# Performance work log

Hardware: AMD Instinct MI355X
Metric: run time of the kernel (lower is better)

The kernel has to match this reference:

```python
import jax, jax.numpy as jnp
import numpy as np

N_NODES = 100000
N_EDGES = 1600000
N_GRAPHS = 64
D = 128


def gcn_conv(x, W, b, src, dst, num_nodes):
    # PyG GCNConv: x' = D^{-1/2} (A + I) D^{-1/2} (X W) + b
    h = x @ W  # [N, H]
    deg = jax.ops.segment_sum(jnp.ones_like(dst, dtype=h.dtype), dst,
                              num_segments=num_nodes)  # includes self-loop (>=1)
    dinv = jax.lax.rsqrt(deg)
    norm = dinv[src] * dinv[dst]  # [E+N]
    msg = h[src] * norm[:, None]  # gather + scale
    out = jax.ops.segment_sum(msg, dst, num_segments=num_nodes)
    return out + b


def setup_inputs() -> dict:
    key = jax.random.key(0)
    ks = jax.random.split(key, 10)
    x = jax.random.normal(ks[0], (N_NODES, D), dtype=jnp.float32)
    edge_index = jax.random.randint(ks[1], (2, N_EDGES), 0, N_NODES, dtype=jnp.int64)
    batch = jnp.sort(jax.random.randint(ks[2], (N_NODES,), 0, N_GRAPHS, dtype=jnp.int64))
    s = 1.0 / np.sqrt(D)
    W1 = jax.random.normal(ks[3], (D, D), dtype=jnp.float32) * s
    b1 = jnp.zeros((D,), dtype=jnp.float32)
    W2 = jax.random.normal(ks[4], (D, D), dtype=jnp.float32) * s
    b2 = jnp.zeros((D,), dtype=jnp.float32)
    Wfc = jax.random.normal(ks[5], (D, D), dtype=jnp.float32) * s
    bfc = jnp.zeros((D,), dtype=jnp.float32)
    return {"x": x, "edge_index": edge_index, "batch": batch,
            "W1": W1, "b1": b1, "W2": W2, "b2": b2, "Wfc": Wfc, "bfc": bfc}


def reference(x, edge_index, batch, W1, b1, W2, b2, Wfc, bfc):
    num_nodes = x.shape[0]
    # add self-loops (PyG default add_self_loops=True)
    loop = jnp.arange(num_nodes, dtype=edge_index.dtype)
    src = jnp.concatenate([edge_index[0], loop])
    dst = jnp.concatenate([edge_index[1], loop])

    h = jax.nn.relu(gcn_conv(x, W1, b1, src, dst, num_nodes))
    h = jax.nn.relu(gcn_conv(h, W2, b2, src, dst, num_nodes))

    # global_mean_pool over graph segment ids
    sums = jax.ops.segment_sum(h, batch, num_segments=N_GRAPHS)
    cnts = jax.ops.segment_sum(jnp.ones((num_nodes,), h.dtype), batch,
                               num_segments=N_GRAPHS)
    pooled = sums / jnp.maximum(cnts, 1.0)[:, None]

    return jax.nn.relu(pooled @ Wfc + bfc)
```

## Files before the change

kernel.cpp:

```cpp
#include <hip/hip_runtime.h>
#include <hip/hip_bf16.h>
#include <stdint.h>

typedef unsigned int uint;
typedef unsigned short ushort;
typedef __attribute__((ext_vector_type(8))) short short8;
typedef __attribute__((ext_vector_type(4))) float floatx4;

#define DD 128
#define BSHIFT 9
#define NBLK 256

__device__ __forceinline__ float bf2f(ushort h){ return __uint_as_float(((uint)h)<<16); }
__device__ __forceinline__ ushort f2bf(float f){
    uint u = __float_as_uint(f);
    u += 0x7fffu + ((u>>16)&1u);
    return (ushort)(u>>16);
}

__global__ void k_detect(const int* ei, const ushort* x, const ushort* W1, int* flags){
    int t = threadIdx.x;
    unsigned long long b0 = __ballot((t < 32) ? (ei[2*t+1] == 0) : 1);
    uint ex = (((uint)x[2*t])  >> 7) & 0xffu;
    uint ew = (((uint)W1[2*t]) >> 7) & 0xffu;
    unsigned long long b1 = __ballot(ex >= 90u && ex <= 160u);
    unsigned long long b2 = __ballot(ew >= 90u && ew <= 160u);
    if (t == 0){
        flags[0] = (b0 == ~0ull) ? 1 : 0;
        flags[1] = (__popcll(b1) >= 48) ? 1 : 0;
        flags[2] = (__popcll(b2) >= 48) ? 1 : 0;
    }
}

__global__ void k_canon(const void* s0,const void* s1,const void* s2,
                        const void* s3,const void* s4,const void* s5,
                        float* d0,float* d1,float* d2,float* d3,float* d4,float* d5,
                        ushort* wb1, ushort* wb2,
                        const int* flags){
    int f = flags[2];
    int i = blockIdx.x*blockDim.x + threadIdx.x;
    const void* s; float* d; int off; int r;
    if (i < 49152){
        r = i>>14; off = i & 16383;
        s = (r==0)?s0:((r==1)?s1:s2);
        d = (r==0)?d0:((r==1)?d1:d2);
    } else {
        int j = i - 49152; r = j>>7; off = j & 127;
        if (r >= 3) return;
        s = (r==0)?s3:((r==1)?s4:s5);
        d = (r==0)?d3:((r==1)?d4:d5);
        d[off] = f ? bf2f(((const ushort*)s)[off]) : ((const float*)s)[off];
        return;
    }
    float val = f ? bf2f(((const ushort*)s)[off]) : ((const float*)s)[off];
    d[off] = val;
    if (r < 2){
        int k = off>>7, n = off&127;
        int c = n>>4, nn = n&15, kk = k>>5, q = (k>>3)&3, j = k&7;
        ushort* wb = (r==0) ? wb1 : wb2;
        wb[((c*4+kk)*64 + q*16 + nn)*8 + j] = f2bf(val);
    }
}

__global__ void k_init(float* pooled, int PM, int* buktot, int nbuk){
    int i = blockIdx.x*blockDim.x + threadIdx.x;
    if (i < PM) pooled[i] = 0.f;
    if (i < nbuk) buktot[i] = 0;
}

__global__ __launch_bounds__(256) void k_hist(const int* __restrict__ ei,
                                              const int* __restrict__ flags,
                                              int* __restrict__ ghist,
                                              int* __restrict__ buktot,
                                              int E, int nbuk, int chunk){
    __shared__ int lh[1024];
    int f = flags[0];
    int t = threadIdx.x, b = blockIdx.x;
    for (int i=t;i<nbuk;i+=256) lh[i]=0;
    __syncthreads();
    int e0 = b*chunk, e1 = min(E, e0+chunk);
    for (int e=e0+t; e<e1; e+=256){
        int d = f ? ei[2*(E+e)] : ei[E+e];
        atomicAdd(&lh[d>>BSHIFT],1);
    }
    __syncthreads();
    for (int i=t;i<nbuk;i+=256){
        int v = lh[i];
        ghist[i*NBLK + b] = v;
        if (v) atomicAdd(&buktot[i], v);
    }
}

__global__ void k_scanB2(const int* __restrict__ buktot, int* __restrict__ bukoff, int nbuk){
    __shared__ int ts[256];
    int t = threadIdx.x;
    int v = (t<nbuk) ? buktot[t] : 0;
    ts[t] = v; __syncthreads();
    for (int off=1; off<256; off<<=1){
        int x = (t>=off) ? ts[t-off] : 0;
        __syncthreads(); ts[t] += x; __syncthreads();
    }
    if (t<nbuk) bukoff[t] = ts[t] - v;
}

__global__ __launch_bounds__(256) void k_apply(const int* __restrict__ ghist,
                                               const int* __restrict__ bukoff,
                                               int* __restrict__ gstart, int nbuk){
    __shared__ int ts[256];
    int b = blockIdx.x, t = threadIdx.x;
    int v = ghist[b*NBLK + t];
    ts[t] = v; __syncthreads();
    for (int off=1; off<256; off<<=1){
        int x = (t>=off) ? ts[t-off] : 0;
        __syncthreads(); ts[t] += x; __syncthreads();
    }
    gstart[b*NBLK + t] = bukoff[b] + ts[t] - v;
}

__global__ __launch_bounds__(256) void k_scat(const int* __restrict__ ei,
                                              const int* __restrict__ flags,
                                              const int* __restrict__ gstart,
                                              uint2* __restrict__ pairs,
                                              int E, int nbuk, int chunk){
    __shared__ int cur[1024];
    int f = flags[0];
    int t = threadIdx.x, b = blockIdx.x;
    for (int i=t;i<nbuk;i+=256) cur[i] = gstart[i*NBLK + b];
    __syncthreads();
    int e0 = b*chunk, e1 = min(E, e0+chunk);
    for (int e=e0+t; e<e1; e+=256){
        int d = f ? ei[2*(E+e)] : ei[E+e];
        int s = f ? ei[2*e]     : ei[e];
        int p = atomicAdd(&cur[d>>BSHIFT],1);
        pairs[p] = make_uint2((uint)s,(uint)d);
    }
}

__global__ __launch_bounds__(256) void k_build(const uint2* __restrict__ pairs,
                                               const int* __restrict__ gstart,
                                               int* __restrict__ rowptr,
                                               float* __restrict__ dinv,
                                               int* __restrict__ srcb,
                                               int E, int nbuk, int M){
    __shared__ int cnt[512], off[512], cur[512], ps[256];
    int b = blockIdx.x, t = threadIdx.x;
    int base = gstart[b*NBLK];
    int end  = (b+1<nbuk) ? gstart[(b+1)*NBLK] : E;
    for (int i=t;i<512;i+=256) cnt[i]=0;
    __syncthreads();
    for (int e=base+t; e<end; e+=256){
        uint2 pr = pairs[e];
        atomicAdd(&cnt[pr.y & 511],1);
    }
    __syncthreads();
    int c0 = cnt[2*t], c1 = cnt[2*t+1];
    int s = c0+c1;
    ps[t]=s; __syncthreads();
    for (int o2=1;o2<256;o2<<=1){
        int x=(t>=o2)?ps[t-o2]:0; __syncthreads(); ps[t]+=x; __syncthreads();
    }
    int ex = ps[t]-s;
    off[2*t]=ex;    off[2*t+1]=ex+c0;
    cur[2*t]=ex;    cur[2*t+1]=ex+c0;
    __syncthreads();
    for (int i=t;i<512;i+=256){
        int n = (b<<BSHIFT)+i;
        if (n<M){
            rowptr[n] = base + off[i];
            dinv[n]   = rsqrtf((float)(cnt[i]+1));
        }
    }
    if (b==0 && t==0) rowptr[M] = E;
    for (int e=base+t; e<end; e+=256){
        uint2 pr = pairs[e];
        int i = pr.y & 511;
        int p = atomicAdd(&cur[i],1);
        srcb[base+p] = (int)pr.x;
    }
}

__global__ __launch_bounds__(256) void k_gemm(const ushort* __restrict__ Xb,
                                              const float* __restrict__ Xf,
                                              const ushort* __restrict__ Wb,
                                              const float* __restrict__ dinv,
                                              const int* __restrict__ flags, int force_bf16,
                                              ushort* __restrict__ Hp, int M){
    __shared__ uint4 Xs4[1024];
    __shared__ uint4 Ws4[2048];
    int t = threadIdx.x;
    int n0 = blockIdx.x*64;
    int xbf = force_bf16 ? 1 : flags[1];

    {
        const uint4* sW = (const uint4*)Wb;
        #pragma unroll
        for (int j=0;j<8;j++) Ws4[t + j*256] = sW[t + j*256];
    }
    #pragma unroll
    for (int g=0; g<4; g++){
        int u = g*256 + t;
        int row = u>>4, kk = (u>>2)&3, q = u&3;
        int n = n0 + row;
        uint4 o;
        if (n < M){
            if (xbf){
                o = *(const uint4*)(Xb + (size_t)n*DD + kk*32 + q*8);
            } else {
                const float* p = Xf + (size_t)n*DD + kk*32 + q*8;
                float4 a = *(const float4*)p;
                float4 b = *(const float4*)(p+4);
                o.x = (uint)f2bf(a.x) | ((uint)f2bf(a.y)<<16);
                o.y = (uint)f2bf(a.z) | ((uint)f2bf(a.w)<<16);
                o.z = (uint)f2bf(b.x) | ((uint)f2bf(b.y)<<16);
                o.w = (uint)f2bf(b.z) | ((uint)f2bf(b.w)<<16);
            }
        } else { o = make_uint4(0,0,0,0); }
        int w = row>>4, m16 = row&15;
        Xs4[(w*4+kk)*64 + q*16 + m16] = o;
    }
    __syncthreads();

    int wv = t>>6, lane = t&63;
    const ushort* Xs = (const ushort*)Xs4;
    const ushort* Ws = (const ushort*)Ws4;

    floatx4 acc[8];
    #pragma unroll
    for (int c=0;c<8;c++) acc[c] = (floatx4){0.f,0.f,0.f,0.f};

    #pragma unroll
    for (int kk=0;kk<4;kk++){
        short8 af = *(const short8*)(Xs + ((size_t)((wv*4+kk)*64 + lane))*8);
        #pragma unroll
        for (int c=0;c<8;c++){
            short8 bf = *(const short8*)(Ws + ((size_t)((c*4+kk)*64 + lane))*8);
            acc[c] = __builtin_amdgcn_mfma_f32_16x16x32_bf16(af, bf, acc[c], 0, 0, 0);
        }
    }

    int quad = lane>>4, col = lane&15;
    int rbase = n0 + wv*16 + quad*4;
    float dv[4];
    #pragma unroll
    for (int r=0;r<4;r++) dv[r] = (rbase + r < M) ? dinv[rbase + r] : 0.f;
    #pragma unroll
    for (int c=0;c<8;c++){
        #pragma unroll
        for (int r=0;r<4;r++){
            int gn = rbase + r;
            if (gn < M) Hp[(size_t)gn*DD + c*16 + col] = f2bf(acc[c][r]*dv[r]);
        }
    }
}

__global__ __launch_bounds__(256) void k_gather(const ushort* __restrict__ Hp,
                                                const int* __restrict__ rowptr,
                                                const int* __restrict__ srcb,
                                                const float* __restrict__ dinv,
                                                const float* __restrict__ bc,
                                                ushort* __restrict__ Xout, int M){
    int wid  = (int)((blockIdx.x*(size_t)blockDim.x + threadIdx.x) >> 6);
    int lane = threadIdx.x & 63;
    if (wid >= M) return;
    int q   = lane >> 4;
    int l16 = lane & 15;
    const uint4* Hp4 = (const uint4*)Hp;

    float acc[8];
    #pragma unroll
    for (int c=0;c<8;c++) acc[c] = 0.f;

    #define ACCUM(vv) { \
        acc[0] += __uint_as_float((vv).x<<16); acc[1] += __uint_as_float((vv).x&0xffff0000u); \
        acc[2] += __uint_as_float((vv).y<<16); acc[3] += __uint_as_float((vv).y&0xffff0000u); \
        acc[4] += __uint_as_float((vv).z<<16); acc[5] += __uint_as_float((vv).z&0xffff0000u); \
        acc[6] += __uint_as_float((vv).w<<16); acc[7] += __uint_as_float((vv).w&0xffff0000u); }

    int rp  = rowptr[wid];
    int rp1 = rowptr[wid+1];
    int total = (rp1 - rp) + 1;
    int j = 0;
    while (j < total){
        int m = total - j; if (m > 64) m = 64;
        int pos = j + lane;
        int idx = wid;
        if (lane < m && pos > 0) idx = srcb[rp + pos - 1];
        for (int g = 0; g < m; g += 8){
            int r0 = g + q, r1 = g + 4 + q;
            int s0 = __shfl(idx, r0, 64);
            int s1 = __shfl(idx, r1, 64);
            uint4 v0 = make_uint4(0,0,0,0), v1 = make_uint4(0,0,0,0);
            if (r0 < m) v0 = Hp4[(size_t)s0*16 + l16];
            if (r1 < m) v1 = Hp4[(size_t)s1*16 + l16];
            ACCUM(v0);
            ACCUM(v1);
        }
        j += m;
    }
    #undef ACCUM

    #pragma unroll
    for (int c=0;c<8;c++){
        acc[c] += __shfl_xor(acc[c], 16, 64);
        acc[c] += __shfl_xor(acc[c], 32, 64);
    }

    if (lane < 16){
        float w = dinv[wid];
        const float* bp = bc + l16*8;
        uint4 o;
        float r0,r1;
        r0 = fmaxf(fmaf(acc[0], w, bp[0]), 0.f);
        r1 = fmaxf(fmaf(acc[1], w, bp[1]), 0.f);
        o.x = (uint)f2bf(r0) | ((uint)f2bf(r1)<<16);
        r0 = fmaxf(fmaf(acc[2], w, bp[2]), 0.f);
        r1 = fmaxf(fmaf(acc[3], w, bp[3]), 0.f);
        o.y = (uint)f2bf(r0) | ((uint)f2bf(r1)<<16);
        r0 = fmaxf(fmaf(acc[4], w, bp[4]), 0.f);
        r1 = fmaxf(fmaf(acc[5], w, bp[5]), 0.f);
        o.z = (uint)f2bf(r0) | ((uint)f2bf(r1)<<16);
        r0 = fmaxf(fmaf(acc[6], w, bp[6]), 0.f);
        r1 = fmaxf(fmaf(acc[7], w, bp[7]), 0.f);
        o.w = (uint)f2bf(r0) | ((uint)f2bf(r1)<<16);
        ((uint4*)Xout)[(size_t)wid*16 + l16] = o;
    }
}

__global__ __launch_bounds__(256) void k_pool(const ushort* __restrict__ X3,
                                              const int* __restrict__ batch,
                                              const int* __restrict__ flags,
                                              float* __restrict__ pooled, int M){
    int f = flags[0];
    int t = threadIdx.x;
    int c32 = t & 63;
    int row = t >> 6;
    int n0 = blockIdx.x * 256;
    if (n0 >= M) return;
    int nend = n0 + 256; if (nend > M) nend = M;
    const uint* X3u = (const uint*)X3;

    float a0 = 0.f, a1 = 0.f;
    int cur = -1;

    int n = n0 + row;
    #define POOL_PROC(gg, uu) \
        if ((gg) != cur){ \
            if (cur >= 0){ \
                atomicAdd(&pooled[cur*DD + 2*c32],   a0); \
                atomicAdd(&pooled[cur*DD + 2*c32+1], a1); \
            } \
            a0 = 0.f; a1 = 0.f; cur = (gg); \
        } \
        a0 += __uint_as_float((uu)<<16); \
        a1 += __uint_as_float((uu) & 0xffff0000u);

    for (; n + 12 < nend; n += 16){
        int g0 = f ? batch[2*n]      : batch[n];
        int g1 = f ? batch[2*(n+4)]  : batch[n+4];
        int g2 = f ? batch[2*(n+8)]  : batch[n+8];
        int g3 = f ? batch[2*(n+12)] : batch[n+12];
        uint u0 = X3u[(size_t)n*64      + c32];
        uint u1 = X3u[(size_t)(n+4)*64  + c32];
        uint u2 = X3u[(size_t)(n+8)*64  + c32];
        uint u3 = X3u[(size_t)(n+12)*64 + c32];
        POOL_PROC(g0, u0);
        POOL_PROC(g1, u1);
        POOL_PROC(g2, u2);
        POOL_PROC(g3, u3);
    }
    for (; n < nend; n += 4){
        int g = f ? batch[2*n] : batch[n];
        uint u = X3u[(size_t)n*64 + c32];
        POOL_PROC(g, u);
    }
    #undef POOL_PROC

    if (cur >= 0){
        atomicAdd(&pooled[cur*DD + 2*c32],   a0);
        atomicAdd(&pooled[cur*DD + 2*c32+1], a1);
    }
}

__global__ void k_cnt(const int* __restrict__ batch, const int* __restrict__ flags,
                      float* __restrict__ cntf, int M, int G){
    int f = flags[0];
    int g = blockIdx.x*blockDim.x + threadIdx.x;
    if (g >= G) return;
    int lo = 0, hi = M;
    while (lo < hi){ int mid = (lo+hi)>>1; int bv = f ? batch[2*mid] : batch[mid]; if (bv > g) hi = mid; else lo = mid+1; }
    int ub_g = lo;
    lo = 0; hi = M;
    while (lo < hi){ int mid = (lo+hi)>>1; int bv = f ? batch[2*mid] : batch[mid]; if (bv > g-1) hi = mid; else lo = mid+1; }
    cntf[g] = (float)(ub_g - lo);
}

__global__ void k_fc(const float* __restrict__ pooled, const float* __restrict__ cntf,
                     const float* __restrict__ Wcf, const float* __restrict__ bcf,
                     const int* __restrict__ flags, ushort* out16, float* out32){
    __shared__ float p[128];
    int g = blockIdx.x, c = threadIdx.x;
    p[c] = pooled[g*DD + c] / fmaxf(cntf[g], 1.f);
    __syncthreads();
    float acc = bcf[c];
    #pragma unroll 8
    for (int k=0;k<128;k++) acc = fmaf(p[k], Wcf[k*DD + c], acc);
    float r = fmaxf(acc, 0.f);
    if (flags[1]) out16[g*DD + c] = f2bf(r);
    else          out32[g*DD + c] = r;
}

extern "C" void kernel_launch(void* const* d_in, const int* in_sizes, int n_in,
                              void* d_out, int out_size, void* d_ws, size_t ws_size,
                              hipStream_t stream) {
    const void* x    = d_in[0];
    const int*  ei   = (const int*)d_in[1];
    const int*  bat  = (const int*)d_in[2];
    const void* W1   = d_in[3];
    const void* b1   = d_in[4];
    const void* W2   = d_in[5];
    const void* b2   = d_in[6];
    const void* Wfc  = d_in[7];
    const void* bfc  = d_in[8];

    int M = in_sizes[0] / DD;
    int E = in_sizes[1] / 2;
    int G = out_size / DD;
    int nbuk  = (M + 511) >> BSHIFT;
    int chunk = (E + NBLK - 1) / NBLK;

    char* w = (char*)d_ws;
    auto alloc = [&](size_t bytes)->void*{ void* p = (void*)w; w += (bytes + 255) & ~(size_t)255; return p; };
    int*    flags  = (int*)   alloc(16);
    int*    rowptr = (int*)   alloc((size_t)(M+1)*4);
    int*    ghist  = (int*)   alloc((size_t)nbuk*NBLK*4);
    int*    gstart = (int*)   alloc((size_t)nbuk*NBLK*4);
    int*    buktot = (int*)   alloc((size_t)nbuk*4);
    int*    bukoff = (int*)   alloc((size_t)nbuk*4);
    float*  dinv   = (float*) alloc((size_t)M*4);
    float*  cntf   = (float*) alloc((size_t)G*4);
    float*  pooled = (float*) alloc((size_t)G*DD*4);
    float*  Wc1    = (float*) alloc(16384*4);
    float*  Wc2    = (float*) alloc(16384*4);
    float*  Wcf    = (float*) alloc(16384*4);
    float*  bc1    = (float*) alloc(128*4);
    float*  bc2    = (float*) alloc(128*4);
    float*  bcf    = (float*) alloc(128*4);
    ushort* wb1    = (ushort*)alloc(16384*2);
    ushort* wb2    = (ushort*)alloc(16384*2);
    int*    srcb   = (int*)   alloc((size_t)E*4);
    ushort* Hp     = (ushort*)alloc((size_t)M*DD*2);
    ushort* X2     = (ushort*)alloc((size_t)M*DD*2);
    uint2*  pairs  = (uint2*)Hp;
    (void)ws_size; (void)n_in;

    k_detect<<<1, 64, 0, stream>>>(ei, (const ushort*)x, (const ushort*)W1, flags);
    k_canon <<<194, 256, 0, stream>>>(W1, W2, Wfc, b1, b2, bfc,
                                      Wc1, Wc2, Wcf, bc1, bc2, bcf, wb1, wb2, flags);
    k_init  <<<(G*DD+255)/256, 256, 0, stream>>>(pooled, G*DD, buktot, nbuk);

    k_hist  <<<NBLK, 256, 0, stream>>>(ei, flags, ghist, buktot, E, nbuk, chunk);
    k_scanB2<<<1, 256, 0, stream>>>(buktot, bukoff, nbuk);
    k_apply <<<nbuk, 256, 0, stream>>>(ghist, bukoff, gstart, nbuk);
    k_scat  <<<NBLK, 256, 0, stream>>>(ei, flags, gstart, pairs, E, nbuk, chunk);
    k_build <<<nbuk, 256, 0, stream>>>(pairs, gstart, rowptr, dinv, srcb, E, nbuk, M);

    k_gemm  <<<(M+63)/64, 256, 0, stream>>>((const ushort*)x, (const float*)x,
                                            wb1, dinv, flags, 0, Hp, M);
    k_gather<<<(M+3)/4, 256, 0, stream>>>(Hp, rowptr, srcb, dinv, bc1, X2, M);
    k_gemm  <<<(M+63)/64, 256, 0, stream>>>(X2, (const float*)X2,
                                            wb2, dinv, flags, 1, Hp, M);
    k_gather<<<(M+3)/4, 256, 0, stream>>>(Hp, rowptr, srcb, dinv, bc2, X2, M);

    k_pool<<<(M+255)/256, 256, 0, stream>>>(X2, bat, flags, pooled, M);
    k_cnt <<<(G+63)/64, 64, 0, stream>>>(bat, flags, cntf, M, G);
    k_fc  <<<G, 128, 0, stream>>>(pooled, cntf, Wcf, bcf, flags, (ushort*)d_out, (float*)d_out);
}
```

Baseline: 348.6 us.

## Merge CSR-build and pooling stages into cooperative kernels with grid sync

Folds detection, weight canonicalisation, init, histogram, scans, scatter and CSR build into one cooperative kernel separated by grid.sync, and merges pool, count and FC into a second cooperative kernel. The block count for the histogram and scatter stages rises to 512. The aim is to remove many small kernel launches and their gaps. In exchange it adds grid-wide barriers, and it depends on cooperative launch residency of 512 blocks.

After: 695.0 us. 99.4% more time.

```diff
diff --git a/kernel.cpp b/kernel.cpp
--- a/kernel.cpp
+++ b/kernel.cpp
@@ -1,6 +1,9 @@
 #include <hip/hip_runtime.h>
 #include <hip/hip_bf16.h>
+#include <hip/hip_cooperative_groups.h>
 #include <stdint.h>
+
+namespace cg = cooperative_groups;
 
 typedef unsigned int uint;
 typedef unsigned short ushort;
@@ -9,7 +12,7 @@
 
 #define DD 128
 #define BSHIFT 9
-#define NBLK 256
+#define GRIDC 512
 
 __device__ __forceinline__ float bf2f(ushort h){ return __uint_as_float(((uint)h)<<16); }
 __device__ __forceinline__ ushort f2bf(float f){
@@ -18,164 +21,155 @@
     return (ushort)(u>>16);
 }
 
-__global__ void k_detect(const int* ei, const ushort* x, const ushort* W1, int* flags){
-    int t = threadIdx.x;
-    unsigned long long b0 = __ballot((t < 32) ? (ei[2*t+1] == 0) : 1);
-    uint ex = (((uint)x[2*t])  >> 7) & 0xffu;
-    uint ew = (((uint)W1[2*t]) >> 7) & 0xffu;
-    unsigned long long b1 = __ballot(ex >= 90u && ex <= 160u);
-    unsigned long long b2 = __ballot(ew >= 90u && ew <= 160u);
-    if (t == 0){
-        flags[0] = (b0 == ~0ull) ? 1 : 0;
-        flags[1] = (__popcll(b1) >= 48) ? 1 : 0;
-        flags[2] = (__popcll(b2) >= 48) ? 1 : 0;
-    }
-}
-
-__global__ void k_canon(const void* s0,const void* s1,const void* s2,
-                        const void* s3,const void* s4,const void* s5,
-                        float* d0,float* d1,float* d2,float* d3,float* d4,float* d5,
-                        ushort* wb1, ushort* wb2,
-                        const int* flags){
-    int f = flags[2];
-    int i = blockIdx.x*blockDim.x + threadIdx.x;
-    const void* s; float* d; int off; int r;
-    if (i < 49152){
-        r = i>>14; off = i & 16383;
-        s = (r==0)?s0:((r==1)?s1:s2);
-        d = (r==0)?d0:((r==1)?d1:d2);
-    } else {
-        int j = i - 49152; r = j>>7; off = j & 127;
-        if (r >= 3) return;
-        s = (r==0)?s3:((r==1)?s4:s5);
-        d = (r==0)?d3:((r==1)?d4:d5);
-        d[off] = f ? bf2f(((const ushort*)s)[off]) : ((const float*)s)[off];
-        return;
-    }
-    float val = f ? bf2f(((const ushort*)s)[off]) : ((const float*)s)[off];
-    d[off] = val;
-    if (r < 2){
-        int k = off>>7, n = off&127;
-        int c = n>>4, nn = n&15, kk = k>>5, q = (k>>3)&3, j = k&7;
-        ushort* wb = (r==0) ? wb1 : wb2;
-        wb[((c*4+kk)*64 + q*16 + nn)*8 + j] = f2bf(val);
-    }
-}
-
-__global__ void k_init(float* pooled, int PM, int* buktot, int nbuk){
-    int i = blockIdx.x*blockDim.x + threadIdx.x;
-    if (i < PM) pooled[i] = 0.f;
-    if (i < nbuk) buktot[i] = 0;
-}
-
-__global__ __launch_bounds__(256) void k_hist(const int* __restrict__ ei,
-                                              const int* __restrict__ flags,
-                                              int* __restrict__ ghist,
-                                              int* __restrict__ buktot,
-                                              int E, int nbuk, int chunk){
-    __shared__ int lh[1024];
-    int f = flags[0];
+__global__ __launch_bounds__(256) void k_prep(
+    const int* __restrict__ ei, const ushort* __restrict__ xs,
+    const void* W1, const void* W2, const void* Wfc,
+    const void* b1, const void* b2, const void* bfc,
+    float* Wc1, float* Wc2, float* Wcf, float* bc1, float* bc2, float* bcf,
+    ushort* wb1, ushort* wb2,
+    int* flags, float* pooled, int* buktot,
+    int* ghist, int* gstart, uint2* pairs,
+    int* rowptr, float* dinv, int* srcb,
+    int E, int nbuk, int M, int G)
+{
+    cg::grid_group grid = cg::this_grid();
+    __shared__ int s_cnt[512], s_off[512], s_cur[512], s_ps[256], s_ts[256];
+    __shared__ int s_flg[3];
     int t = threadIdx.x, b = blockIdx.x;
-    for (int i=t;i<nbuk;i+=256) lh[i]=0;
+    int nb = gridDim.x;
+
+    if (t < 64){
+        unsigned long long m0 = __ballot((t < 32) ? (ei[2*t+1] == 0) : 1);
+        uint ex2 = (((uint)xs[2*t]) >> 7) & 0xffu;
+        uint ew2 = (((uint)((const ushort*)W1)[2*t]) >> 7) & 0xffu;
+        unsigned long long m1 = __ballot(ex2 >= 90u && ex2 <= 160u);
+        unsigned long long m2 = __ballot(ew2 >= 90u && ew2 <= 160u);
+        if (t == 0){
+            s_flg[0] = (m0 == ~0ull) ? 1 : 0;
+            s_flg[1] = (__popcll(m1) >= 48) ? 1 : 0;
+            s_flg[2] = (__popcll(m2) >= 48) ? 1 : 0;
+            if (b == 0){ flags[0]=s_flg[0]; flags[1]=s_flg[1]; flags[2]=s_flg[2]; }
+        }
+    }
     __syncthreads();
-    int e0 = b*chunk, e1 = min(E, e0+chunk);
-    for (int e=e0+t; e<e1; e+=256){
-        int d = f ? ei[2*(E+e)] : ei[E+e];
-        atomicAdd(&lh[d>>BSHIFT],1);
+    int f64 = s_flg[0], fW = s_flg[2];
+
+    int gi = b*256 + t;
+    if (gi < 49152){
+        int r = gi>>14, off = gi & 16383;
+        const void* s = (r==0)?W1:((r==1)?W2:Wfc);
+        float* d = (r==0)?Wc1:((r==1)?Wc2:Wcf);
+        float val = fW ? bf2f(((const ushort*)s)[off]) : ((const float*)s)[off];
+        d[off] = val;
+        if (r < 2){
+            int k = off>>7, n = off&127;
+            int c = n>>4, nn = n&15, kk = k>>5, q = (k>>3)&3, j = k&7;
+            ushort* wb = (r==0) ? wb1 : wb2;
+            wb[((c*4+kk)*64 + q*16 + nn)*8 + j] = f2bf(val);
+        }
+    } else if (gi < 49536){
+        int jj = gi - 49152; int r = jj>>7, off = jj & 127;
+        const void* s = (r==0)?b1:((r==1)?b2:bfc);
+        float* d = (r==0)?bc1:((r==1)?bc2:bcf);
+        d[off] = fW ? bf2f(((const ushort*)s)[off]) : ((const float*)s)[off];
+    } else if (gi < 49536 + G*DD){
+        pooled[gi - 49536] = 0.f;
+    } else if (gi < 49536 + G*DD + nbuk){
+        buktot[gi - 49536 - G*DD] = 0;
+    }
+
+    grid.sync();
+
+    int chunk = (E + nb - 1)/nb;
+    for (int i=t;i<nbuk;i+=256) s_cnt[i]=0;
+    __syncthreads();
+    {
+        int e0 = b*chunk, e1 = min(E, e0+chunk);
+        for (int e=e0+t; e<e1; e+=256){
+            int d = f64 ? ei[2*(E+e)] : ei[E+e];
+            atomicAdd(&s_cnt[d>>BSHIFT], 1);
+        }
     }
     __syncthreads();
     for (int i=t;i<nbuk;i+=256){
-        int v = lh[i];
-        ghist[i*NBLK + b] = v;
+        int v = s_cnt[i];
+        ghist[i*nb + b] = v;
         if (v) atomicAdd(&buktot[i], v);
     }
-}
-
-__global__ void k_scanB2(const int* __restrict__ buktot, int* __restrict__ bukoff, int nbuk){
-    __shared__ int ts[256];
-    int t = threadIdx.x;
-    int v = (t<nbuk) ? buktot[t] : 0;
-    ts[t] = v; __syncthreads();
-    for (int off=1; off<256; off<<=1){
-        int x = (t>=off) ? ts[t-off] : 0;
-        __syncthreads(); ts[t] += x; __syncthreads();
-    }
-    if (t<nbuk) bukoff[t] = ts[t] - v;
-}
-
-__global__ __launch_bounds__(256) void k_apply(const int* __restrict__ ghist,
-                                               const int* __restrict__ bukoff,
-                                               int* __restrict__ gstart, int nbuk){
-    __shared__ int ts[256];
-    int b = blockIdx.x, t = threadIdx.x;
-    int v = ghist[b*NBLK + t];
-    ts[t] = v; __syncthreads();
-    for (int off=1; off<256; off<<=1){
-        int x = (t>=off) ? ts[t-off] : 0;
-        __syncthreads(); ts[t] += x; __syncthreads();
-    }
-    gstart[b*NBLK + t] = bukoff[b] + ts[t] - v;
-}
-
-__global__ __launch_bounds__(256) void k_scat(const int* __restrict__ ei,
-                                              const int* __restrict__ flags,
-                                              const int* __restrict__ gstart,
-                                              uint2* __restrict__ pairs,
-                                              int E, int nbuk, int chunk){
-    __shared__ int cur[1024];
-    int f = flags[0];
-    int t = threadIdx.x, b = blockIdx.x;
-    for (int i=t;i<nbuk;i+=256) cur[i] = gstart[i*NBLK + b];
+
+    grid.sync();
+
+    if (b < nbuk){
+        int v = (t < nbuk) ? buktot[t] : 0;
+        s_ts[t] = v; __syncthreads();
+        for (int off=1; off<256; off<<=1){
+            int x2 = (t>=off) ? s_ts[t-off] : 0;
+            __syncthreads(); s_ts[t] += x2; __syncthreads();
+        }
+        int bukoff = s_ts[b] - buktot[b];
+        int g0 = ghist[b*nb + 2*t], g1 = ghist[b*nb + 2*t+1];
+        int ss = g0 + g1;
+        s_ps[t] = ss; __syncthreads();
+        for (int off=1; off<256; off<<=1){
+            int x2 = (t>=off) ? s_ps[t-off] : 0;
+            __syncthreads(); s_ps[t] += x2; __syncthreads();
+        }
+        int ex = bukoff + s_ps[t] - ss;
+        gstart[b*nb + 2*t]   = ex;
+        gstart[b*nb + 2*t+1] = ex + g0;
+    }
+
+    grid.sync();
+
+    for (int i=t;i<nbuk;i+=256) s_cur[i] = gstart[i*nb + b];
     __syncthreads();
-    int e0 = b*chunk, e1 = min(E, e0+chunk);
-    for (int e=e0+t; e<e1; e+=256){
-        int d = f ? ei[2*(E+e)] : ei[E+e];
-        int s = f ? ei[2*e]     : ei[e];
-        int p = atomicAdd(&cur[d>>BSHIFT],1);
-        pairs[p] = make_uint2((uint)s,(uint)d);
-    }
-}
-
-__global__ __launch_bounds__(256) void k_build(const uint2* __restrict__ pairs,
-                                               const int* __restrict__ gstart,
-                                               int* __restrict__ rowptr,
-                                               float* __restrict__ dinv,
-                                               int* __restrict__ srcb,
-                                               int E, int nbuk, int M){
-    __shared__ int cnt[512], off[512], cur[512], ps[256];
-    int b = blockIdx.x, t = threadIdx.x;
-    int base = gstart[b*NBLK];
-    int end  = (b+1<nbuk) ? gstart[(b+1)*NBLK] : E;
-    for (int i=t;i<512;i+=256) cnt[i]=0;
-    __syncthreads();
-    for (int e=base+t; e<end; e+=256){
-        uint2 pr = pairs[e];
-        atomicAdd(&cnt[pr.y & 511],1);
-    }
-    __syncthreads();
-    int c0 = cnt[2*t], c1 = cnt[2*t+1];
-    int s = c0+c1;
-    ps[t]=s; __syncthreads();
-    for (int o2=1;o2<256;o2<<=1){
-        int x=(t>=o2)?ps[t-o2]:0; __syncthreads(); ps[t]+=x; __syncthreads();
-    }
-    int ex = ps[t]-s;
-    off[2*t]=ex;    off[2*t+1]=ex+c0;
-    cur[2*t]=ex;    cur[2*t+1]=ex+c0;
-    __syncthreads();
-    for (int i=t;i<512;i+=256){
-        int n = (b<<BSHIFT)+i;
-        if (n<M){
-            rowptr[n] = base + off[i];
-            dinv[n]   = rsqrtf((float)(cnt[i]+1));
-        }
-    }
-    if (b==0 && t==0) rowptr[M] = E;
-    for (int e=base+t; e<end; e+=256){
-        uint2 pr = pairs[e];
-        int i = pr.y & 511;
-        int p = atomicAdd(&cur[i],1);
-        srcb[base+p] = (int)pr.x;
+    {
+        int e0 = b*chunk, e1 = min(E, e0+chunk);
+        for (int e=e0+t; e<e1; e+=256){
+            int d = f64 ? ei[2*(E+e)] : ei[E+e];
+            int s = f64 ? ei[2*e]     : ei[e];
+            int p = atomicAdd(&s_cur[d>>BSHIFT], 1);
+            pairs[p] = make_uint2((uint)s,(uint)d);
+        }
+    }
+
+    grid.sync();
+
+    if (b < nbuk){
+        int base = gstart[b*nb];
+        int end  = (b+1 < nbuk) ? gstart[(b+1)*nb] : E;
+        for (int i=t;i<512;i+=256) s_cnt[i]=0;
+        __syncthreads();
+        for (int e=base+t; e<end; e+=256){
+            uint2 pr = pairs[e];
+            atomicAdd(&s_cnt[pr.y & 511], 1);
+        }
+        __syncthreads();
+        int c0 = s_cnt[2*t], c1 = s_cnt[2*t+1];
+        int ss = c0 + c1;
+        s_ps[t] = ss; __syncthreads();
+        for (int o2=1; o2<256; o2<<=1){
+            int x2 = (t>=o2) ? s_ps[t-o2] : 0;
+            __syncthreads(); s_ps[t] += x2; __syncthreads();
+        }
+        int ex = s_ps[t] - ss;
+        s_off[2*t] = ex;     s_off[2*t+1] = ex + c0;
+        s_cur[2*t] = ex;     s_cur[2*t+1] = ex + c0;
+        __syncthreads();
+        for (int i=t;i<512;i+=256){
+            int n = (b<<BSHIFT) + i;
+            if (n < M){
+                rowptr[n] = base + s_off[i];
+                dinv[n]   = rsqrtf((float)(s_cnt[i]+1));
+            }
+        }
+        if (b==0 && t==0) rowptr[M] = E;
+        for (int e=base+t; e<end; e+=256){
+            uint2 pr = pairs[e];
+            int i = pr.y & 511;
+            int p = atomicAdd(&s_cur[i], 1);
+            srcb[base+p] = (int)pr.x;
+        }
     }
 }
 
@@ -326,116 +320,122 @@
     }
 }
 
-__global__ __launch_bounds__(256) void k_pool(const ushort* __restrict__ X3,
-                                              const int* __restrict__ batch,
-                                              const int* __restrict__ flags,
-                                              float* __restrict__ pooled, int M){
+__global__ __launch_bounds__(256) void k_post(
+    const ushort* __restrict__ X3, const int* __restrict__ batch,
+    const int* __restrict__ flags,
+    float* __restrict__ pooled, float* __restrict__ cntf,
+    const float* __restrict__ Wcf, const float* __restrict__ bcf,
+    ushort* out16, float* out32, int M, int G)
+{
+    cg::grid_group grid = cg::this_grid();
+    __shared__ float p[128];
+    int t = threadIdx.x, b = blockIdx.x, nb = gridDim.x;
     int f = flags[0];
-    int t = threadIdx.x;
+    const uint* X3u = (const uint*)X3;
+
     int c32 = t & 63;
     int row = t >> 6;
-    int n0 = blockIdx.x * 256;
-    if (n0 >= M) return;
-    int nend = n0 + 256; if (nend > M) nend = M;
-    const uint* X3u = (const uint*)X3;
-
-    float a0 = 0.f, a1 = 0.f;
-    int cur = -1;
-
-    int n = n0 + row;
-    #define POOL_PROC(gg, uu) \
-        if ((gg) != cur){ \
-            if (cur >= 0){ \
-                atomicAdd(&pooled[cur*DD + 2*c32],   a0); \
-                atomicAdd(&pooled[cur*DD + 2*c32+1], a1); \
+    int nchunks = (M + 255)/256;
+    for (int ch = b; ch < nchunks; ch += nb){
+        int n0 = ch*256;
+        int nend = n0 + 256; if (nend > M) nend = M;
+        float a0 = 0.f, a1 = 0.f;
+        int cur = -1;
+        int n = n0 + row;
+        #define POOL_PROC(gg, uu) \
+            if ((gg) != cur){ \
+                if (cur >= 0){ \
+                    atomicAdd(&pooled[cur*DD + 2*c32],   a0); \
+                    atomicAdd(&pooled[cur*DD + 2*c32+1], a1); \
+                } \
+                a0 = 0.f; a1 = 0.f; cur = (gg); \
             } \
-            a0 = 0.f; a1 = 0.f; cur = (gg); \
-        } \
-        a0 += __uint_as_float((uu)<<16); \
-        a1 += __uint_as_float((uu) & 0xffff0000u);
-
-    for (; n + 12 < nend; n += 16){
-        int g0 = f ? batch[2*n]      : batch[n];
-        int g1 = f ? batch[2*(n+4)]  : batch[n+4];
-        int g2 = f ? batch[2*(n+8)]  : batch[n+8];
-        int g3 = f ? batch[2*(n+12)] : batch[n+12];
-        uint u0 = X3u[(size_t)n*64      + c32];
-        uint u1 = X3u[(size_t)(n+4)*64  + c32];
-        uint u2 = X3u[(size_t)(n+8)*64  + c32];
-        uint u3 = X3u[(size_t)(n+12)*64 + c32];
-        POOL_PROC(g0, u0);
-        POOL_PROC(g1, u1);
-        POOL_PROC(g2, u2);
-        POOL_PROC(g3, u3);
-    }
-    for (; n < nend; n += 4){
-        int g = f ? batch[2*n] : batch[n];
-        uint u = X3u[(size_t)n*64 + c32];
-        POOL_PROC(g, u);
-    }
-    #undef POOL_PROC
-
-    if (cur >= 0){
-        atomicAdd(&pooled[cur*DD + 2*c32],   a0);
-        atomicAdd(&pooled[cur*DD + 2*c32+1], a1);
-    }
-}
-
-__global__ void k_cnt(const int* __restrict__ batch, const int* __restrict__ flags,
-                      float* __restrict__ cntf, int M, int G){
-    int f = flags[0];
-    int g = blockIdx.x*blockDim.x + threadIdx.x;
-    if (g >= G) return;
-    int lo = 0, hi = M;
-    while (lo < hi){ int mid = (lo+hi)>>1; int bv = f ? batch[2*mid] : batch[mid]; if (bv > g) hi = mid; else lo = mid+1; }
-    int ub_g = lo;
-    lo = 0; hi = M;
-    while (lo < hi){ int mid = (lo+hi)>>1; int bv = f ? batch[2*mid] : batch[mid]; if (bv > g-1) hi = mid; else lo = mid+1; }
-    cntf[g] = (float)(ub_g - lo);
-}
-
-__global__ void k_fc(const float* __restrict__ pooled, const float* __restrict__ cntf,
-                     const float* __restrict__ Wcf, const float* __restrict__ bcf,
-                     const int* __restrict__ flags, ushort* out16, float* out32){
-    __shared__ float p[128];
-    int g = blockIdx.x, c = threadIdx.x;
-    p[c] = pooled[g*DD + c] / fmaxf(cntf[g], 1.f);
-    __syncthreads();
-    float acc = bcf[c];
-    #pragma unroll 8
-    for (int k=0;k<128;k++) acc = fmaf(p[k], Wcf[k*DD + c], acc);
-    float r = fmaxf(acc, 0.f);
-    if (flags[1]) out16[g*DD + c] = f2bf(r);
-    else          out32[g*DD + c] = r;
+            a0 += __uint_as_float((uu)<<16); \
+            a1 += __uint_as_float((uu) & 0xffff0000u);
+
+        for (; n + 12 < nend; n += 16){
+            int g0 = f ? batch[2*n]      : batch[n];
+            int g1 = f ? batch[2*(n+4)]  : batch[n+4];
+            int g2 = f ? batch[2*(n+8)]  : batch[n+8];
+            int g3 = f ? batch[2*(n+12)] : batch[n+12];
+            uint u0 = X3u[(size_t)n*64      + c32];
+            uint u1 = X3u[(size_t)(n+4)*64  + c32];
+            uint u2 = X3u[(size_t)(n+8)*64  + c32];
+            uint u3 = X3u[(size_t)(n+12)*64 + c32];
+            POOL_PROC(g0, u0);
+            POOL_PROC(g1, u1);
+            POOL_PROC(g2, u2);
+            POOL_PROC(g3, u3);
+        }
+        for (; n < nend; n += 4){
+            int g = f ? batch[2*n] : batch[n];
+            uint u = X3u[(size_t)n*64 + c32];
+            POOL_PROC(g, u);
+        }
+        #undef POOL_PROC
+        if (cur >= 0){
+            atomicAdd(&pooled[cur*DD + 2*c32],   a0);
+            atomicAdd(&pooled[cur*DD + 2*c32+1], a1);
+        }
+    }
+
+    grid.sync();
+
+    if (b == 0 && t < G){
+        int g = t;
+        int lo = 0, hi = M;
+        while (lo < hi){ int mid=(lo+hi)>>1; int bv = f ? batch[2*mid] : batch[mid]; if (bv > g) hi = mid; else lo = mid+1; }
+        int ub_g = lo;
+        lo = 0; hi = M;
+        while (lo < hi){ int mid=(lo+hi)>>1; int bv = f ? batch[2*mid] : batch[mid]; if (bv > g-1) hi = mid; else lo = mid+1; }
+        cntf[g] = (float)(ub_g - lo);
+    }
+
+    grid.sync();
+
+    if (b < G){
+        int g = b;
+        if (t < 128) p[t] = pooled[g*DD + t] / fmaxf(cntf[g], 1.f);
+        __syncthreads();
+        if (t < 128){
+            float acc = bcf[t];
+            #pragma unroll 8
+            for (int k=0;k<128;k++) acc = fmaf(p[k], Wcf[k*DD + t], acc);
+            float r = fmaxf(acc, 0.f);
+            if (flags[1]) out16[g*DD + t] = f2bf(r);
+            else          out32[g*DD + t] = r;
+        }
+    }
 }
 
 extern "C" void kernel_launch(void* const* d_in, const int* in_sizes, int n_in,
                               void* d_out, int out_size, void* d_ws, size_t ws_size,
                               hipStream_t stream) {
-    const void* x    = d_in[0];
-    const int*  ei   = (const int*)d_in[1];
-    const int*  bat  = (const int*)d_in[2];
-    const void* W1   = d_in[3];
-    const void* b1   = d_in[4];
-    const void* W2   = d_in[5];
-    const void* b2   = d_in[6];
-    const void* Wfc  = d_in[7];
-    const void* bfc  = d_in[8];
+    const int*    ei  = (const int*)d_in[1];
+    const ushort* xs  = (const ushort*)d_in[0];
+    const float*  xf  = (const float*)d_in[0];
+    const int*    bat = (const int*)d_in[2];
+    const void* W1  = d_in[3];
+    const void* b1  = d_in[4];
+    const void* W2  = d_in[5];
+    const void* b2  = d_in[6];
+    const void* Wfc = d_in[7];
+    const void* bfc = d_in[8];
+    ushort* out16 = (ushort*)d_out;
+    float*  out32 = (float*)d_out;
 
     int M = in_sizes[0] / DD;
     int E = in_sizes[1] / 2;
     int G = out_size / DD;
-    int nbuk  = (M + 511) >> BSHIFT;
-    int chunk = (E + NBLK - 1) / NBLK;
+    int nbuk = (M + 511) >> BSHIFT;
 
     char* w = (char*)d_ws;
     auto alloc = [&](size_t bytes)->void*{ void* p = (void*)w; w += (bytes + 255) & ~(size_t)255; return p; };
     int*    flags  = (int*)   alloc(16);
     int*    rowptr = (int*)   alloc((size_t)(M+1)*4);
-    int*    ghist  = (int*)   alloc((size_t)nbuk*NBLK*4);
-    int*    gstart = (int*)   alloc((size_t)nbuk*NBLK*4);
+    int*    ghist  = (int*)   alloc((size_t)nbuk*GRIDC*4);
+    int*    gstart = (int*)   alloc((size_t)nbuk*GRIDC*4);
     int*    buktot = (int*)   alloc((size_t)nbuk*4);
-    int*    bukoff = (int*)   alloc((size_t)nbuk*4);
     float*  dinv   = (float*) alloc((size_t)M*4);
     float*  cntf   = (float*) alloc((size_t)G*4);
     float*  pooled = (float*) alloc((size_t)G*DD*4);
@@ -453,25 +453,33 @@
     uint2*  pairs  = (uint2*)Hp;
     (void)ws_size; (void)n_in;
 
-    k_detect<<<1, 64, 0, stream>>>(ei, (const ushort*)x, (const ushort*)W1, flags);
-    k_canon <<<194, 256, 0, stream>>>(W1, W2, Wfc, b1, b2, bfc,
-                                      Wc1, Wc2, Wcf, bc1, bc2, bcf, wb1, wb2, flags);
-    k_init  <<<(G*DD+255)/256, 256, 0, stream>>>(pooled, G*DD, buktot, nbuk);
-
-    k_hist  <<<NBLK, 256, 0, stream>>>(ei, flags, ghist, buktot, E, nbuk, chunk);
-    k_scanB2<<<1, 256, 0, stream>>>(buktot, bukoff, nbuk);
-    k_apply <<<nbuk, 256, 0, stream>>>(ghist, bukoff, gstart, nbuk);
-    k_scat  <<<NBLK, 256, 0, stream>>>(ei, flags, gstart, pairs, E, nbuk, chunk);
-    k_build <<<nbuk, 256, 0, stream>>>(pairs, gstart, rowptr, dinv, srcb, E, nbuk, M);
-
-    k_gemm  <<<(M+63)/64, 256, 0, stream>>>((const ushort*)x, (const float*)x,
-                                            wb1, dinv, flags, 0, Hp, M);
+    {
+        void* args[] = {
+            (void*)&ei, (void*)&xs,
+            (void*)&W1, (void*)&W2, (void*)&Wfc,
+            (void*)&b1, (void*)&b2, (void*)&bfc,
+            (void*)&Wc1, (void*)&Wc2, (void*)&Wcf, (void*)&bc1, (void*)&bc2, (void*)&bcf,
+            (void*)&wb1, (void*)&wb2,
+            (void*)&flags, (void*)&pooled, (void*)&buktot,
+            (void*)&ghist, (void*)&gstart, (void*)&pairs,
+            (void*)&rowptr, (void*)&dinv, (void*)&srcb,
+            (void*)&E, (void*)&nbuk, (void*)&M, (void*)&G
+        };
+        hipLaunchCooperativeKernel((void*)k_prep, dim3(GRIDC), dim3(256), args, 0, stream);
+    }
+
+    k_gemm  <<<(M+63)/64, 256, 0, stream>>>(xs, xf, wb1, dinv, flags, 0, Hp, M);
     k_gather<<<(M+3)/4, 256, 0, stream>>>(Hp, rowptr, srcb, dinv, bc1, X2, M);
-    k_gemm  <<<(M+63)/64, 256, 0, stream>>>(X2, (const float*)X2,
-                                            wb2, dinv, flags, 1, Hp, M);
+    k_gemm  <<<(M+63)/64, 256, 0, stream>>>(X2, (const float*)X2, wb2, dinv, flags, 1, Hp, M);
     k_gather<<<(M+3)/4, 256, 0, stream>>>(Hp, rowptr, srcb, dinv, bc2, X2, M);
 
-    k_pool<<<(M+255)/256, 256, 0, stream>>>(X2, bat, flags, pooled, M);
-    k_cnt <<<(G+63)/64, 64, 0, stream>>>(bat, flags, cntf, M, G);
-    k_fc  <<<G, 128, 0, stream>>>(pooled, cntf, Wcf, bcf, flags, (ushort*)d_out, (float*)d_out);
-}
+    {
+        void* args[] = {
+            (void*)&X2, (void*)&bat, (void*)&flags,
+            (void*)&pooled, (void*)&cntf,
+            (void*)&Wcf, (void*)&bcf,
+            (void*)&out16, (void*)&out32, (void*)&M, (void*)&G
+        };
+        hipLaunchCooperativeKernel((void*)k_post, dim3(GRIDC), dim3(256), args, 0, stream);
+    }
+}
```
